# Optimization experiments

Hardware: AMD Instinct MI355X
Metric: run time of the kernel (lower is better)

Reference implementation:

```python
import jax, jax.numpy as jnp
import numpy as np

NUM_HEADS = 8
WINDOW = 5


def local_mask(T, w):
    # non-causal band: attend iff |i - j| <= w
    i = jnp.arange(T)
    return jnp.abs(i[:, None] - i[None, :]) <= w


def setup_inputs() -> dict:
    key = jax.random.key(0)
    k1, k2, k3 = jax.random.split(key, 3)
    B, T, S, C = 2, 64, 1024, 512  # batch, frames, spatial (32x32), hidden
    x = jax.random.normal(k1, (B, T * S, C), dtype=jnp.float32)
    W_qkv = jax.random.normal(k2, (C, 3 * C), dtype=jnp.float32) * (C ** -0.5)
    W_out = jax.random.normal(k3, (C, C), dtype=jnp.float32) * (C ** -0.5)
    return {"x": x, "W_qkv": W_qkv, "W_out": W_out, "num_frames": T}


def reference(x, W_qkv, W_out, num_frames):
    B, N, C = x.shape
    H = NUM_HEADS
    hd = C // H
    T = num_frames
    S = N // T
    scale = hd ** -0.5

    qkv = (x @ W_qkv).reshape(B, T, S, 3, H, hd)
    q = qkv[:, :, :, 0]  # [B,T,S,H,hd]
    k = qkv[:, :, :, 1]
    v = qkv[:, :, :, 2]

    # temporal attention: independent per (batch, head, spatial location)
    scores = jnp.einsum('btshd,bushd->bhstu', q, k) * scale  # [B,H,S,T,T]
    mask = local_mask(T, WINDOW)  # [T,T]
    scores = jnp.where(mask[None, None, None], scores, -jnp.inf)
    attn = jax.nn.softmax(scores, axis=-1)
    out = jnp.einsum('bhstu,bushd->btshd', attn, v)  # [B,T,S,H,hd]
    out = out.reshape(B, N, C) @ W_out
    return out
```

## Files before the change

kernel.cpp:

```cpp
#include <hip/hip_runtime.h>
#include <stdint.h>

#define B_   2
#define T_   64
#define S_   1024
#define C_   512
#define H_   8
#define N_   (T_ * S_)
#define M_   (B_ * N_)
#define WIN_ 5

typedef unsigned short u16;
typedef __bf16 bf16;
typedef __bf16 bf16x8 __attribute__((ext_vector_type(8)));
typedef float  f32x4  __attribute__((ext_vector_type(4)));
typedef u16    u16x8  __attribute__((ext_vector_type(8)));

static __device__ __forceinline__ u16 f2bf(float f) {
    return __builtin_bit_cast(u16, (bf16)f);
}
static __device__ __forceinline__ float bf2f(u16 u) {
    return __builtin_bit_cast(float, (uint32_t)u << 16);
}
static __device__ __forceinline__ void gload16(const void* g, void* l) {
    __builtin_amdgcn_global_load_lds(
        (const __attribute__((address_space(1))) void*)g,
        (__attribute__((address_space(3))) void*)l, 16, 0, 0);
}
static __device__ __forceinline__ long permute_row(long grow) {
    int b = (int)(grow >> 16);
    int t = (int)(grow >> 10) & 63;
    int s = (int)grow & 1023;
    return ((long)((b << 10) | s)) * 64 + t;
}


__global__ __launch_bounds__(256) void prep_w(const float* __restrict__ W,
                                              u16* __restrict__ WT, int NCOL) {
    int id = blockIdx.x * 256 + threadIdx.x;
    int n  = id % NCOL;
    int gi = id / NCOL;
    int chunk = gi >> 2;
    int g     = gi & 3;
    int k0 = chunk * 32 + g * 8;
    int cs = chunk ^ ((n >> 3) & 1);
    int gs = g ^ ((n >> 1) & 3);
    u16x8 w;
    #pragma unroll
    for (int j = 0; j < 8; ++j) w[j] = f2bf(W[(size_t)(k0 + j) * NCOL + n]);
    *(u16x8*)&WT[(size_t)n * 512 + cs * 32 + gs * 8] = w;
}

__global__ __launch_bounds__(256) void prep_w2(const float* __restrict__ W,
                                               u16* __restrict__ WT2) {
    int id = blockIdx.x * 256 + threadIdx.x;
    int n  = id % 1536;
    int gi = id / 1536;
    int chunk = gi >> 2;
    int g     = gi & 3;
    int k0 = chunk * 32 + g * 8;
    int which = n >> 9;
    int h     = (n >> 6) & 7;
    int d     = n & 63;
    int rloc  = which * 64 + d;
    long np   = h * 192 + rloc;
    int cs = chunk ^ ((rloc >> 3) & 1);
    int gs = g ^ ((rloc >> 1) & 3);
    u16x8 w;
    #pragma unroll
    for (int j = 0; j < 8; ++j) w[j] = f2bf(W[(size_t)(k0 + j) * 1536 + n]);
    *(u16x8*)&WT2[(size_t)np * 512 + cs * 32 + gs * 8] = w;
}

__global__ __launch_bounds__(256) void prep_x(const float* __restrict__ x,
                                              u16* __restrict__ xb) {
    const size_t total = (size_t)M_ * 64;
    for (size_t id = (size_t)blockIdx.x * 256 + threadIdx.x; id < total;
         id += (size_t)gridDim.x * 256) {
        long r_in = (long)(id >> 6);
        int  gi   = (int)(id & 63);
        int chunk = gi >> 2;
        int g     = gi & 3;
        long rid  = permute_row(r_in);
        int cb  = (int)(rid >> 3) & 1;
        int key = (int)(rid >> 1) & 3;
        const float* src = x + r_in * 512 + chunk * 32 + g * 8;
        f32x4 v0 = *(const f32x4*)(src);
        f32x4 v1 = *(const f32x4*)(src + 4);
        u16x8 w;
        #pragma unroll
        for (int j = 0; j < 4; ++j) { w[j] = f2bf(v0[j]); w[4 + j] = f2bf(v1[j]); }
        *(u16x8*)&xb[(size_t)rid * 512 + (chunk ^ cb) * 32 + ((g ^ key) << 3)] = w;
    }
}

#define LDF(off) __builtin_bit_cast(bf16x8, *(const u16x8*)&lds[(off)])
#define MFMA16(d, a, b) d = __builtin_amdgcn_mfma_f32_16x16x32_bf16(a, b, d, 0, 0, 0)

#define PSTR 200

__global__ __launch_bounds__(512, 2) void gemm_attn(const u16* __restrict__ Ap,
                                                    const u16* __restrict__ Bp,
                                                    u16* __restrict__ attn) {
    __shared__ u16 lds[57344];

    const int tid  = threadIdx.x;
    const int lane = tid & 63;
    const int wid  = tid >> 6;
    const int wm   = wid >> 1;
    const int wn   = wid & 1;
    const int fr   = lane & 15;
    const int g0   = lane >> 4;

    const int rowtile = ((blockIdx.x >> 6) << 3) | (blockIdx.x & 7);
    const int h       = (blockIdx.x >> 3) & 7;
    const long row0   = (long)rowtile * 256;

    int aoffs[4], boffs[6];
    #pragma unroll
    for (int mf = 0; mf < 4; ++mf) {
        int lr = wm * 64 + mf * 16 + fr;
        aoffs[mf] = lr * 64 + (((lr >> 3) & 1) << 5) + (((g0 ^ (lr >> 1)) & 3) << 3);
    }
    #pragma unroll
    for (int nf = 0; nf < 6; ++nf) {
        int lc = wn * 96 + nf * 16 + fr;
        boffs[nf] = lc * 64 + (((lc >> 3) & 1) << 5) + (((g0 ^ (lc >> 1)) & 3) << 3);
    }

    const int srow = lane >> 3;
    const int scol = (lane & 7) * 8;

    auto stageA = [&](int tt, int half) {
        const int ab = (tt & 1) * 16384;
        #pragma unroll
        for (int i = 0; i < 2; ++i) {
            int r = half * 128 + i * 64 + wid * 8 + srow;
            const u16* g = Ap + (row0 + r) * 512 + tt * 64 + scol;
            gload16(g, (void*)&lds[ab + r * 64]);
        }
    };
    auto stageB = [&](int tt) {
        const int bb = 32768 + (tt & 1) * 12288;
        #pragma unroll
        for (int i = 0; i < 3; ++i) {
            int r = i * 64 + wid * 8 + srow;
            const u16* g = Bp + (size_t)(h * 192 + r) * 512 + tt * 64 + scol;
            gload16(g, (void*)&lds[bb + r * 64]);
        }
    };

    f32x4 acc[4][6] = {};

    stageA(0, 0); stageA(0, 1); stageB(0); stageB(1);
    asm volatile("s_waitcnt vmcnt(3)" ::: "memory");
    __builtin_amdgcn_sched_barrier(0);
    __builtin_amdgcn_s_barrier();

    #pragma unroll
    for (int t = 0; t < 8; ++t) {
        const int ab = (t & 1) * 16384;
        const int bb = 32768 + (t & 1) * 12288;
        bf16x8 af0[4], af1[4], bf0[6], bf1[6];
        #pragma unroll
        for (int mf = 0; mf < 4; ++mf) af0[mf] = LDF(ab + aoffs[mf]);
        #pragma unroll
        for (int nf = 0; nf < 3; ++nf) bf0[nf] = LDF(bb + boffs[nf]);
        if (t <= 6) stageA(t + 1, 0);
        __builtin_amdgcn_s_barrier();
        asm volatile("s_waitcnt lgkmcnt(0)" ::: "memory");
        __builtin_amdgcn_sched_barrier(0);
        __builtin_amdgcn_s_setprio(1);
        #pragma unroll
        for (int mf = 0; mf < 4; ++mf) {
            MFMA16(acc[mf][0], af0[mf], bf0[0]);
            MFMA16(acc[mf][1], af0[mf], bf0[1]);
            MFMA16(acc[mf][2], af0[mf], bf0[2]);
        }
        __builtin_amdgcn_s_setprio(0);
        __builtin_amdgcn_s_barrier();
        #pragma unroll
        for (int nf = 3; nf < 6; ++nf) bf0[nf] = LDF(bb + boffs[nf]);
        if (t <= 6) stageA(t + 1, 1);
        __builtin_amdgcn_s_barrier();
        asm volatile("s_waitcnt lgkmcnt(0)" ::: "memory");
        __builtin_amdgcn_sched_barrier(0);
        __builtin_amdgcn_s_setprio(1);
        #pragma unroll
        for (int mf = 0; mf < 4; ++mf) {
            MFMA16(acc[mf][3], af0[mf], bf0[3]);
            MFMA16(acc[mf][4], af0[mf], bf0[4]);
            MFMA16(acc[mf][5], af0[mf], bf0[5]);
        }
        __builtin_amdgcn_s_setprio(0);
        __builtin_amdgcn_s_barrier();
        #pragma unroll
        for (int mf = 0; mf < 4; ++mf) af1[mf] = LDF(ab + (aoffs[mf] ^ 32));
        #pragma unroll
        for (int nf = 0; nf < 6; ++nf) bf1[nf] = LDF(bb + (boffs[nf] ^ 32));
        __builtin_amdgcn_s_barrier();
        asm volatile("s_waitcnt lgkmcnt(0)" ::: "memory");
        __builtin_amdgcn_sched_barrier(0);
        __builtin_amdgcn_s_setprio(1);
        #pragma unroll
        for (int mf = 0; mf < 4; ++mf) {
            MFMA16(acc[mf][0], af1[mf], bf1[0]);
            MFMA16(acc[mf][1], af1[mf], bf1[1]);
            MFMA16(acc[mf][2], af1[mf], bf1[2]);
        }
        __builtin_amdgcn_s_setprio(0);
        __builtin_amdgcn_s_barrier();
        if (t <= 5) stageB(t + 2);
        __builtin_amdgcn_s_barrier();
        __builtin_amdgcn_s_setprio(1);
        #pragma unroll
        for (int mf = 0; mf < 4; ++mf) {
            MFMA16(acc[mf][3], af1[mf], bf1[3]);
            MFMA16(acc[mf][4], af1[mf], bf1[4]);
            MFMA16(acc[mf][5], af1[mf], bf1[5]);
        }
        __builtin_amdgcn_s_setprio(0);
        if (t <= 5) {
            asm volatile("s_waitcnt vmcnt(3)" ::: "memory");
        } else if (t == 6) {
            asm volatile("s_waitcnt vmcnt(0)" ::: "memory");
        }
        __builtin_amdgcn_sched_barrier(0);
        __builtin_amdgcn_s_barrier();
    }

    __builtin_amdgcn_sched_barrier(0);
    #pragma unroll
    for (int mf = 0; mf < 4; ++mf) {
        #pragma unroll
        for (int nf = 0; nf < 6; ++nf) {
            #pragma unroll
            for (int r = 0; r < 4; ++r) {
                int row = wm * 64 + mf * 16 + (lane >> 4) * 4 + r;
                int col = wn * 96 + nf * 16 + fr;
                lds[row * PSTR + col] = f2bf(acc[mf][nf][r]);
            }
        }
    }
    __syncthreads();

    if (wid < 4) {
        const int slab = wid;
        const int t = lane;
        const int prow = slab * 64 + t;
        float qf[64];
        #pragma unroll
        for (int c = 0; c < 8; ++c) {
            u16x8 v = *(const u16x8*)&lds[prow * PSTR + c * 8];
            #pragma unroll
            for (int j = 0; j < 8; ++j) qf[c * 8 + j] = bf2f(v[j]);
        }
        float p[11];
        float m = -1e30f;
        #pragma unroll
        for (int i = 0; i < 11; ++i) {
            int u = t - WIN_ + i;
            if (u >= 0 && u < 64) {
                const int ub = (slab * 64 + u) * PSTR + 64;
                float dot = 0.f;
                #pragma unroll
                for (int c = 0; c < 8; ++c) {
                    u16x8 kv = *(const u16x8*)&lds[ub + c * 8];
                    #pragma unroll
                    for (int j = 0; j < 8; ++j) dot += qf[c * 8 + j] * bf2f(kv[j]);
                }
                p[i] = dot * 0.125f;
                m = fmaxf(m, p[i]);
            } else {
                p[i] = -1e30f;
            }
        }
        float sum = 0.f;
        #pragma unroll
        for (int i = 0; i < 11; ++i) {
            int u = t - WIN_ + i;
            float e = (u >= 0 && u < 64) ? __expf(p[i] - m) : 0.f;
            p[i] = e;
            sum += e;
        }
        const float inv = 1.f / sum;
        float o[64];
        #pragma unroll
        for (int d = 0; d < 64; ++d) o[d] = 0.f;
        #pragma unroll
        for (int i = 0; i < 11; ++i) {
            int u = t - WIN_ + i;
            if (u >= 0 && u < 64) {
                const int ub = (slab * 64 + u) * PSTR + 128;
                float pv = p[i] * inv;
                #pragma unroll
                for (int c = 0; c < 8; ++c) {
                    u16x8 vv = *(const u16x8*)&lds[ub + c * 8];
                    #pragma unroll
                    for (int j = 0; j < 8; ++j) o[c * 8 + j] += pv * bf2f(vv[j]);
                }
            }
        }
        long rid = row0 + prow;
        int s = (int)(rid >> 6) & 1023;
        size_t rowbase = (size_t)rid * C_;
        const int cb  = (s >> 3) & 1;
        const int key = (s >> 1) & 3;
        #pragma unroll
        for (int c = 0; c < 8; ++c) {
            u16x8 w;
            #pragma unroll
            for (int j = 0; j < 8; ++j) w[j] = f2bf(o[c * 8 + j]);
            int off = (((2 * h + (c >> 2)) ^ cb) << 5) + (((c & 3) ^ key) << 3);
            *(u16x8*)&attn[rowbase + off] = w;
        }
    }
}

template<int NCOL, bool OUT_BF16, bool A_PERM>
__global__ __launch_bounds__(512, 2) void gemm8_k(const u16* __restrict__ Ap,
                                                  const u16* __restrict__ Bp,
                                                  void* __restrict__ Dp, int gx) {
    __shared__ u16 lds[65536];

    const int tid  = threadIdx.x;
    const int lane = tid & 63;
    const int wid  = tid >> 6;
    const int wm   = wid >> 2;
    const int wn   = wid & 3;
    const int fr   = lane & 15;
    const int g0   = lane >> 4;

    const int nwg = gridDim.x;
    const int q8  = nwg >> 3;
    const int bid = blockIdx.x;
    const int wg  = (bid & 7) * q8 + (bid >> 3);
    const int bx  = wg % gx;
    const int by  = wg / gx;
    const long row0 = (long)by * 256;
    const int  col0 = bx * 256;

    int aoffs[8], boffs[4];
    #pragma unroll
    for (int mf = 0; mf < 8; ++mf) {
        int lr = wm * 128 + mf * 16 + fr;
        aoffs[mf] = lr * 64 + (((lr >> 3) & 1) << 5) + (((g0 ^ (lr >> 1)) & 3) << 3);
    }
    #pragma unroll
    for (int nf = 0; nf < 4; ++nf) {
        int lc = wn * 64 + nf * 16 + fr;
        boffs[nf] = lc * 64 + (((lc >> 3) & 1) << 5) + (((g0 ^ (lc >> 1)) & 3) << 3);
    }

    const int srow = lane >> 3;
    const int scol = (lane & 7) * 8;

    long arow_phys[4];
    #pragma unroll
    for (int half = 0; half < 2; ++half)
        #pragma unroll
        for (int i = 0; i < 2; ++i) {
            int r = half * 128 + i * 64 + wid * 8 + srow;
            long grow = row0 + r;
            arow_phys[half * 2 + i] = A_PERM ? permute_row(grow) : grow;
        }

    auto stageA = [&](int tt, int half) {
        const int ab = (tt & 1) * 32768;
        #pragma unroll
        for (int i = 0; i < 2; ++i) {
            int r = half * 128 + i * 64 + wid * 8 + srow;
            const u16* g = Ap + arow_phys[half * 2 + i] * 512 + tt * 64 + scol;
            gload16(g, (void*)&lds[ab + r * 64]);
        }
    };
    auto stageB = [&](int tt, int half) {
        const int ab = (tt & 1) * 32768;
        #pragma unroll
        for (int i = 0; i < 2; ++i) {
            int r = half * 128 + i * 64 + wid * 8 + srow;
            const u16* g = Bp + (size_t)(col0 + r) * 512 + tt * 64 + scol;
            gload16(g, (void*)&lds[ab + 16384 + r * 64]);
        }
    };

    f32x4 acc[8][4] = {};

    stageA(0, 0); stageA(0, 1); stageB(0, 0); stageB(0, 1);
    stageB(1, 0); stageB(1, 1);
    asm volatile("s_waitcnt vmcnt(4)" ::: "memory");
    __builtin_amdgcn_sched_barrier(0);
    __builtin_amdgcn_s_barrier();

    #pragma unroll
    for (int t = 0; t < 8; ++t) {
        const int ab = (t & 1) * 32768;
        bf16x8 af0[8], af1[8], bf0[4], bf1[4];
        #pragma unroll
        for (int mf = 0; mf < 4; ++mf) af0[mf] = LDF(ab + aoffs[mf]);
        #pragma unroll
        for (int nf = 0; nf < 4; ++nf) bf0[nf] = LDF(ab + 16384 + boffs[nf]);
        if (t <= 6) stageA(t + 1, 0);
        __builtin_amdgcn_s_barrier();
        asm volatile("s_waitcnt lgkmcnt(0)" ::: "memory");
        __builtin_amdgcn_sched_barrier(0);
        __builtin_amdgcn_s_setprio(1);
        #pragma unroll
        for (int mf = 0; mf < 4; ++mf) {
            MFMA16(acc[mf][0], af0[mf], bf0[0]);
            MFMA16(acc[mf][1], af0[mf], bf0[1]);
            MFMA16(acc[mf][2], af0[mf], bf0[2]);
            MFMA16(acc[mf][3], af0[mf], bf0[3]);
        }
        __builtin_amdgcn_s_setprio(0);
        __builtin_amdgcn_s_barrier();
        #pragma unroll
        for (int mf = 4; mf < 8; ++mf) af0[mf] = LDF(ab + aoffs[mf]);
        #pragma unroll
        for (int nf = 0; nf < 4; ++nf) bf1[nf] = LDF(ab + 16384 + (boffs[nf] ^ 32));
        if (t <= 6) stageA(t + 1, 1);
        __builtin_amdgcn_s_barrier();
        asm volatile("s_waitcnt lgkmcnt(0)" ::: "memory");
        __builtin_amdgcn_sched_barrier(0);
        __builtin_amdgcn_s_setprio(1);
        #pragma unroll
        for (int mf = 4; mf < 8; ++mf) {
            MFMA16(acc[mf][0], af0[mf], bf0[0]);
            MFMA16(acc[mf][1], af0[mf], bf0[1]);
            MFMA16(acc[mf][2], af0[mf], bf0[2]);
            MFMA16(acc[mf][3], af0[mf], bf0[3]);
        }
        __builtin_amdgcn_s_setprio(0);
        __builtin_amdgcn_s_barrier();
        #pragma unroll
        for (int mf = 0; mf < 4; ++mf) af1[mf] = LDF(ab + (aoffs[mf] ^ 32));
        if (t <= 5) stageB(t + 2, 0);
        __builtin_amdgcn_s_barrier();
        asm volatile("s_waitcnt lgkmcnt(0)" ::: "memory");
        __builtin_amdgcn_sched_barrier(0);
        __builtin_amdgcn_s_setprio(1);
        #pragma unroll
        for (int mf = 0; mf < 4; ++mf) {
            MFMA16(acc[mf][0], af1[mf], bf1[0]);
            MFMA16(acc[mf][1], af1[mf], bf1[1]);
            MFMA16(acc[mf][2], af1[mf], bf1[2]);
            MFMA16(acc[mf][3], af1[mf], bf1[3]);
        }
        __builtin_amdgcn_s_setprio(0);
        __builtin_amdgcn_s_barrier();
        #pragma unroll
        for (int mf = 4; mf < 8; ++mf) af1[mf] = LDF(ab + (aoffs[mf] ^ 32));
        if (t <= 5) stageB(t + 2, 1);
        __builtin_amdgcn_s_barrier();
        asm volatile("s_waitcnt lgkmcnt(0)" ::: "memory");
        __builtin_amdgcn_sched_barrier(0);
        __builtin_amdgcn_s_setprio(1);
        #pragma unroll
        for (int mf = 4; mf < 8; ++mf) {
            MFMA16(acc[mf][0], af1[mf], bf1[0]);
            MFMA16(acc[mf][1], af1[mf], bf1[1]);
            MFMA16(acc[mf][2], af1[mf], bf1[2]);
            MFMA16(acc[mf][3], af1[mf], bf1[3]);
        }
        __builtin_amdgcn_s_setprio(0);
        if (t <= 5) {
            asm volatile("s_waitcnt vmcnt(4)" ::: "memory");
        } else if (t == 6) {
            asm volatile("s_waitcnt vmcnt(0)" ::: "memory");
        }
        __builtin_amdgcn_sched_barrier(0);
        __builtin_amdgcn_s_barrier();
    }

    #pragma unroll
    for (int mf = 0; mf < 8; ++mf) {
        #pragma unroll
        for (int nf = 0; nf < 4; ++nf) {
            #pragma unroll
            for (int r = 0; r < 4; ++r) {
                long grow = row0 + wm * 128 + mf * 16 + (lane >> 4) * 4 + r;
                int  gcol = col0 + wn * 64 + nf * 16 + fr;
                float v = acc[mf][nf][r];
                if constexpr (OUT_BF16) ((u16*)Dp)[grow * NCOL + gcol] = f2bf(v);
                else                    ((float*)Dp)[grow * NCOL + gcol] = v;
            }
        }
    }
}

extern "C" void kernel_launch(void* const* d_in, const int* in_sizes, int n_in,
                              void* d_out, int out_size, void* d_ws, size_t ws_size,
                              hipStream_t stream) {
    const float* x    = (const float*)d_in[0];
    const float* Wqkv = (const float*)d_in[1];
    const float* Wout = (const float*)d_in[2];
    float* out = (float*)d_out;

    const size_t xc_elems = (size_t)M_ * C_;
    u16* xb       = (u16*)d_ws;
    u16* attn_buf = xb + xc_elems;
    u16* WqkvT2   = attn_buf + xc_elems;
    u16* WoutT    = WqkvT2 + (size_t)1536 * 512;
    if (ws_size < ((size_t)(WoutT + (size_t)512 * 512) - (size_t)d_ws)) return;

    prep_w2<<<(1536 * 64) / 256, 256, 0, stream>>>(Wqkv, WqkvT2);
    prep_w<<<(512 * 64) / 256, 256, 0, stream>>>(Wout, WoutT, 512);
    prep_x<<<8192, 256, 0, stream>>>(x, xb);

    gemm_attn<<<4096, 512, 0, stream>>>(xb, WqkvT2, attn_buf);

    gemm8_k<512, false, true><<<1024, 512, 0, stream>>>(attn_buf, WoutT, (void*)out, 2);
}
```

Baseline: 530.5 us.

## Halve fused QKV-attention row tile to 128 rows and raise occupancy

The fused QKV GEMM plus temporal-attention kernel now processes 128 rows per block instead of 256. The 8 waves are rearranged as 2x4 over a 128x192 tile, and the grid doubles to 8192 blocks. LDS use drops so launch bounds can ask for 4 blocks per CU, and the inner k-loop is simplified to two phases with fewer MFMA groups. Each weight slice is now reloaded twice as often, only 2 of 8 waves do the attention epilogue, and there is less MFMA work per barrier to hide latency.

```diff
diff --git a/kernel.cpp b/kernel.cpp
--- a/kernel.cpp
+++ b/kernel.cpp
@@ -99,32 +99,32 @@
 
 #define PSTR 200
 
-__global__ __launch_bounds__(512, 2) void gemm_attn(const u16* __restrict__ Ap,
+__global__ __launch_bounds__(512, 4) void gemm_attn(const u16* __restrict__ Ap,
                                                     const u16* __restrict__ Bp,
                                                     u16* __restrict__ attn) {
-    __shared__ u16 lds[57344];
+    __shared__ u16 lds[40960];
 
     const int tid  = threadIdx.x;
     const int lane = tid & 63;
     const int wid  = tid >> 6;
-    const int wm   = wid >> 1;
-    const int wn   = wid & 1;
+    const int wm   = wid >> 2;
+    const int wn   = wid & 3;
     const int fr   = lane & 15;
     const int g0   = lane >> 4;
 
     const int rowtile = ((blockIdx.x >> 6) << 3) | (blockIdx.x & 7);
     const int h       = (blockIdx.x >> 3) & 7;
-    const long row0   = (long)rowtile * 256;
-
-    int aoffs[4], boffs[6];
+    const long row0   = (long)rowtile * 128;
+
+    int aoffs[4], boffs[3];
     #pragma unroll
     for (int mf = 0; mf < 4; ++mf) {
         int lr = wm * 64 + mf * 16 + fr;
         aoffs[mf] = lr * 64 + (((lr >> 3) & 1) << 5) + (((g0 ^ (lr >> 1)) & 3) << 3);
     }
     #pragma unroll
-    for (int nf = 0; nf < 6; ++nf) {
-        int lc = wn * 96 + nf * 16 + fr;
+    for (int nf = 0; nf < 3; ++nf) {
+        int lc = wn * 48 + nf * 16 + fr;
         boffs[nf] = lc * 64 + (((lc >> 3) & 1) << 5) + (((g0 ^ (lc >> 1)) & 3) << 3);
     }
 
@@ -132,16 +132,13 @@
     const int scol = (lane & 7) * 8;
 
     auto stageA = [&](int tt, int half) {
-        const int ab = (tt & 1) * 16384;
-        #pragma unroll
-        for (int i = 0; i < 2; ++i) {
-            int r = half * 128 + i * 64 + wid * 8 + srow;
-            const u16* g = Ap + (row0 + r) * 512 + tt * 64 + scol;
-            gload16(g, (void*)&lds[ab + r * 64]);
-        }
+        const int ab = (tt & 1) * 8192;
+        int r = half * 64 + wid * 8 + srow;
+        const u16* g = Ap + (row0 + r) * 512 + tt * 64 + scol;
+        gload16(g, (void*)&lds[ab + r * 64]);
     };
     auto stageB = [&](int tt) {
-        const int bb = 32768 + (tt & 1) * 12288;
+        const int bb = 16384 + (tt & 1) * 12288;
         #pragma unroll
         for (int i = 0; i < 3; ++i) {
             int r = i * 64 + wid * 8 + srow;
@@ -150,7 +147,7 @@
         }
     };
 
-    f32x4 acc[4][6] = {};
+    f32x4 acc[4][3] = {};
 
     stageA(0, 0); stageA(0, 1); stageB(0); stageB(1);
     asm volatile("s_waitcnt vmcnt(3)" ::: "memory");
@@ -159,92 +156,70 @@
 
     #pragma unroll
     for (int t = 0; t < 8; ++t) {
-        const int ab = (t & 1) * 16384;
-        const int bb = 32768 + (t & 1) * 12288;
-        bf16x8 af0[4], af1[4], bf0[6], bf1[6];
-        #pragma unroll
-        for (int mf = 0; mf < 4; ++mf) af0[mf] = LDF(ab + aoffs[mf]);
-        #pragma unroll
-        for (int nf = 0; nf < 3; ++nf) bf0[nf] = LDF(bb + boffs[nf]);
-        if (t <= 6) stageA(t + 1, 0);
+        const int ab = (t & 1) * 8192;
+        const int bb = 16384 + (t & 1) * 12288;
+        bf16x8 af[4], bfv[3];
+        #pragma unroll
+        for (int mf = 0; mf < 4; ++mf) af[mf] = LDF(ab + aoffs[mf]);
+        #pragma unroll
+        for (int nf = 0; nf < 3; ++nf) bfv[nf] = LDF(bb + boffs[nf]);
+        if (t <= 6) { stageA(t + 1, 0); stageA(t + 1, 1); }
         __builtin_amdgcn_s_barrier();
         asm volatile("s_waitcnt lgkmcnt(0)" ::: "memory");
         __builtin_amdgcn_sched_barrier(0);
         __builtin_amdgcn_s_setprio(1);
         #pragma unroll
         for (int mf = 0; mf < 4; ++mf) {
-            MFMA16(acc[mf][0], af0[mf], bf0[0]);
-            MFMA16(acc[mf][1], af0[mf], bf0[1]);
-            MFMA16(acc[mf][2], af0[mf], bf0[2]);
-        }
-        __builtin_amdgcn_s_setprio(0);
-        __builtin_amdgcn_s_barrier();
-        #pragma unroll
-        for (int nf = 3; nf < 6; ++nf) bf0[nf] = LDF(bb + boffs[nf]);
-        if (t <= 6) stageA(t + 1, 1);
+            MFMA16(acc[mf][0], af[mf], bfv[0]);
+            MFMA16(acc[mf][1], af[mf], bfv[1]);
+            MFMA16(acc[mf][2], af[mf], bfv[2]);
+        }
+        __builtin_amdgcn_s_setprio(0);
+        __builtin_amdgcn_s_barrier();
+        #pragma unroll
+        for (int mf = 0; mf < 4; ++mf) af[mf] = LDF(ab + (aoffs[mf] ^ 32));
+        #pragma unroll
+        for (int nf = 0; nf < 3; ++nf) bfv[nf] = LDF(bb + (boffs[nf] ^ 32));
         __builtin_amdgcn_s_barrier();
         asm volatile("s_waitcnt lgkmcnt(0)" ::: "memory");
         __builtin_amdgcn_sched_barrier(0);
         __builtin_amdgcn_s_setprio(1);
         #pragma unroll
         for (int mf = 0; mf < 4; ++mf) {
-            MFMA16(acc[mf][3], af0[mf], bf0[3]);
-            MFMA16(acc[mf][4], af0[mf], bf0[4]);
-            MFMA16(acc[mf][5], af0[mf], bf0[5]);
-        }
-        __builtin_amdgcn_s_setprio(0);
-        __builtin_amdgcn_s_barrier();
-        #pragma unroll
-        for (int mf = 0; mf < 4; ++mf) af1[mf] = LDF(ab + (aoffs[mf] ^ 32));
-        #pragma unroll
-        for (int nf = 0; nf < 6; ++nf) bf1[nf] = LDF(bb + (boffs[nf] ^ 32));
-        __builtin_amdgcn_s_barrier();
-        asm volatile("s_waitcnt lgkmcnt(0)" ::: "memory");
-        __builtin_amdgcn_sched_barrier(0);
-        __builtin_amdgcn_s_setprio(1);
-        #pragma unroll
-        for (int mf = 0; mf < 4; ++mf) {
-            MFMA16(acc[mf][0], af1[mf], bf1[0]);
-            MFMA16(acc[mf][1], af1[mf], bf1[1]);
-            MFMA16(acc[mf][2], af1[mf], bf1[2]);
-        }
-        __builtin_amdgcn_s_setprio(0);
-        __builtin_amdgcn_s_barrier();
-        if (t <= 5) stageB(t + 2);
-        __builtin_amdgcn_s_barrier();
-        __builtin_amdgcn_s_setprio(1);
-        #pragma unroll
-        for (int mf = 0; mf < 4; ++mf) {
-            MFMA16(acc[mf][3], af1[mf], bf1[3]);
-            MFMA16(acc[mf][4], af1[mf], bf1[4]);
-            MFMA16(acc[mf][5], af1[mf], bf1[5]);
-        }
-        __builtin_amdgcn_s_setprio(0);
-        if (t <= 5) {
-            asm volatile("s_waitcnt vmcnt(3)" ::: "memory");
-        } else if (t == 6) {
-            asm volatile("s_waitcnt vmcnt(0)" ::: "memory");
-        }
-        __builtin_amdgcn_sched_barrier(0);
-        __builtin_amdgcn_s_barrier();
+            MFMA16(acc[mf][0], af[mf], bfv[0]);
+            MFMA16(acc[mf][1], af[mf], bfv[1]);
+            MFMA16(acc[mf][2], af[mf], bfv[2]);
+        }
+        __builtin_amdgcn_s_setprio(0);
+        __builtin_amdgcn_s_barrier();
+        if (t <= 6) {
+            if (t <= 5) {
+                stageB(t + 2);
+                asm volatile("s_waitcnt vmcnt(3)" ::: "memory");
+            } else {
+                asm volatile("s_waitcnt vmcnt(0)" ::: "memory");
+            }
+            __builtin_amdgcn_sched_barrier(0);
+            __builtin_amdgcn_s_barrier();
+        }
     }
 
     __builtin_amdgcn_sched_barrier(0);
     #pragma unroll
     for (int mf = 0; mf < 4; ++mf) {
         #pragma unroll
-        for (int nf = 0; nf < 6; ++nf) {
+        for (int nf = 0; nf < 3; ++nf) {
             #pragma unroll
             for (int r = 0; r < 4; ++r) {
                 int row = wm * 64 + mf * 16 + (lane >> 4) * 4 + r;
-                int col = wn * 96 + nf * 16 + fr;
+                int col = wn * 48 + nf * 16 + fr;
                 lds[row * PSTR + col] = f2bf(acc[mf][nf][r]);
             }
         }
     }
     __syncthreads();
 
-    if (wid < 4) {
+    if (wid < 2) {
         const int slab = wid;
         const int t = lane;
         const int prow = slab * 64 + t;
@@ -507,7 +482,7 @@
     prep_w<<<(512 * 64) / 256, 256, 0, stream>>>(Wout, WoutT, 512);
     prep_x<<<8192, 256, 0, stream>>>(x, xb);
 
-    gemm_attn<<<4096, 512, 0, stream>>>(xb, WqkvT2, attn_buf);
+    gemm_attn<<<8192, 512, 0, stream>>>(xb, WqkvT2, attn_buf);
 
     gemm8_k<512, false, true><<<1024, 512, 0, stream>>>(attn_buf, WoutT, (void*)out, 2);
 }
```

New measurement: 510.6 us. 3.7% less time.
